# Optimization experiments

Hardware: AMD Instinct MI355X
Metric: run time of the kernel (lower is better)

The kernel has to match this reference:

```python
import jax, jax.numpy as jnp
import numpy as np


def setup_inputs() -> dict:
    key = jax.random.key(0)
    B, C, H, W = 8, 512, 64, 64
    x = jax.random.normal(key, (B, C, H, W), dtype=jnp.float32)
    # flag: 1 = masked (hole) position, 0 = known. Center-square hole as in
    # mask to this resolution; with shift_sz=1, mask_thred=1 flag == mask).
    flag = np.zeros((H, W), dtype=np.int32)
    flag[H // 4: 3 * H // 4, W // 4: 3 * W // 4] = 1
    return {"input": x, "flag": jnp.asarray(flag)}


def reference(input, flag):
    B, C, H, W = input.shape
    c2 = C // 2
    hw = H * W
    former = input[:, :c2]          # decoder features (B, c2, H, W)
    latter = input[:, c2:]          # encoder features (B, c2, H, W)

    ff = former.reshape(B, c2, hw)  # (B, c2, P)
    lf = latter.reshape(B, c2, hw)  # (B, c2, P)

    # L2-normalize latter pixel features (shift_sz=1 patches == pixels);
    # matches util.cosine_similarity's normalized conv kernels.
    norms = jnp.linalg.norm(lf, axis=1, keepdims=True)
    lnorm = lf / jnp.maximum(norms, 1e-8)

    # cosine[b, p, q] = <former[b,:,p], normed_latter[b,:,q]> for all positions;
    # masked q are excluded from the argmax (equiv. to gathering only the
    # non-mask patches via nonmask_point_idx, but jit-friendly fixed shapes).
    cos = jnp.einsum('bcp,bcq->bpq', ff, lnorm)
    flag_f = flag.reshape(hw)
    neg_inf = jnp.asarray(-jnp.inf, cos.dtype)
    cos = jnp.where(flag_f[None, None, :] == 1, neg_inf, cos)

    idx = jnp.argmax(cos, axis=2)   # (B, P): best non-mask source per position

    # Gather RAW latter features at best-match positions (util.shift_offsets
    # applies the 0/1 transition matrix ind_lst to the un-normalized latter).
    gidx = jnp.broadcast_to(idx[:, None, :], (B, c2, hw))
    shift = jnp.take_along_axis(lf, gidx, axis=2)            # (B, c2, P)
    shift = jnp.where(flag_f[None, None, :] == 1, shift, 0.0)  # zeros at known px
    shift = shift.reshape(B, c2, H, W)

    return jnp.concatenate([former, latter, shift], axis=1)   # (B, 3*c2, H, W)
```

## Files before the change

kernel.cpp:

```cpp
#include <hip/hip_runtime.h>
#include <stdint.h>
#include <math.h>

#define HW   4096
#define NB   8
#define NC   512
#define C2   256
#define PT   32
#define QC   512

#define WS_PACKED 0
#define WS_INVN   262144
#define WS_Q0     393216
#define WS_P1     409600
#define WS_CNT    425984
#define WS_IDX    427008
#define WS_INVC   558080

__device__ __forceinline__ unsigned long long mkkey(float v, unsigned q) {
    unsigned u = __float_as_uint(v);
    u = (u & 0x80000000u) ? ~u : (u | 0x80000000u);
    return ((unsigned long long)u << 32) | (unsigned long long)(0xFFFFFFFFu - q);
}

__device__ __forceinline__ float* lfc_region(float* out, int b) {
    return out + ((size_t)b * 768 + 512) * HW;
}

__global__ void compact_kernel(const int* __restrict__ flag, int* __restrict__ q0,
                               int* __restrict__ p1, int* __restrict__ cnt) {
    __shared__ int c1s[256];
    int t = threadIdx.x;
    int f[16]; int n1 = 0;
    #pragma unroll
    for (int j = 0; j < 16; ++j) { f[j] = flag[t*16 + j]; n1 += (f[j] == 1); }
    c1s[t] = n1;
    __syncthreads();
    if (t == 0) {
        int run = 0;
        for (int i = 0; i < 256; ++i) { int v = c1s[i]; c1s[i] = run; run += v; }
        cnt[0] = run;
        cnt[1] = HW - run;
    }
    __syncthreads();
    int b1 = c1s[t];
    int b0 = t*16 - c1s[t];
    for (int j = 0; j < 16; ++j) {
        int i = t*16 + j;
        if (f[j] == 1) p1[b1++] = i; else q0[b0++] = i;
    }
}

__global__ void norm_kernel(const float* __restrict__ x, float* __restrict__ invn) {
    int b = blockIdx.y;
    int q = blockIdx.x * 256 + threadIdx.x;
    const float* lf = x + ((size_t)b * NC + C2) * HW + q;
    float s = 0.f;
    #pragma unroll 8
    for (int c = 0; c < C2; ++c) {
        float v = lf[c * HW];
        s = fmaf(v, v, s);
    }
    invn[b * HW + q] = 1.0f / fmaxf(sqrtf(s), 1e-8f);
}

__global__ void pack_kernel(const float* __restrict__ x, const float* __restrict__ invn,
                            const int* __restrict__ q0, const int* __restrict__ cnt,
                            float* __restrict__ out, float* __restrict__ invc) {
    int b = blockIdx.z, c = blockIdx.y;
    int n0 = cnt[1];
    int ns = (n0 + 3) & ~3;
    int k = blockIdx.x * 256 + threadIdx.x;
    if (k >= n0) return;
    int q = q0[k];
    float* lfc = lfc_region(out, b);
    lfc[(size_t)c * ns + k] = x[((size_t)b * NC + C2 + c) * HW + q];
    if (c == 0) invc[b * HW + k] = invn[b * HW + q];
}

__global__ void __launch_bounds__(256) argmax_kernel(
        const float* __restrict__ x, float* __restrict__ out,
        const float* __restrict__ invc,
        const int* __restrict__ q0, const int* __restrict__ p1,
        const int* __restrict__ cnt, unsigned long long* __restrict__ packed) {
    int tile  = blockIdx.x;
    int chunk = blockIdx.y;
    int b     = blockIdx.z;
    int n1 = cnt[0], n0 = cnt[1];
    if (tile * PT >= n1) return;
    if (chunk * QC >= n0) return;
    int ns = (n0 + 3) & ~3;

    __shared__ float sff[256][PT];
    __shared__ int   sp[PT];

    int t = threadIdx.x;
    if (t < PT) sp[t] = (tile * PT + t < n1) ? p1[tile * PT + t] : -1;
    __syncthreads();

    const float* xb = x + (size_t)b * NC * HW;
    #pragma unroll
    for (int k = 0; k < 32; ++k) {
        int i = t + (k << 8);
        int c = i >> 5, j = i & 31;
        int p = sp[j];
        sff[c][j] = (p >= 0) ? xb[c * HW + p] : 0.f;
    }
    __syncthreads();

    int tp = t >> 6;
    int tq = t & 63;
    const float* lfc = lfc_region(out, b);
    int kbase = chunk * QC + tq * 4;

    const float* r = lfc + kbase;
    float4 bv0 = *(const float4*)(r);
    float4 bv1 = *(const float4*)(r + 256);
    r += ns;

    float acc[8][8];
    #pragma unroll
    for (int pi = 0; pi < 8; ++pi)
        #pragma unroll
        for (int j = 0; j < 8; ++j) acc[pi][j] = 0.f;

    #pragma unroll 2
    for (int c = 0; c < 255; ++c) {
        float4 nb0 = *(const float4*)(r);
        float4 nb1 = *(const float4*)(r + 256);
        r += ns;
        const float4* arow = (const float4*)&sff[c][tp * 8];
        float4 a0 = arow[0], a1 = arow[1];
        float av[8] = {a0.x, a0.y, a0.z, a0.w, a1.x, a1.y, a1.z, a1.w};
        float bv[8] = {bv0.x, bv0.y, bv0.z, bv0.w, bv1.x, bv1.y, bv1.z, bv1.w};
        #pragma unroll
        for (int pi = 0; pi < 8; ++pi)
            #pragma unroll
            for (int j = 0; j < 8; ++j)
                acc[pi][j] = fmaf(av[pi], bv[j], acc[pi][j]);
        bv0 = nb0; bv1 = nb1;
    }
    {
        const float4* arow = (const float4*)&sff[255][tp * 8];
        float4 a0 = arow[0], a1 = arow[1];
        float av[8] = {a0.x, a0.y, a0.z, a0.w, a1.x, a1.y, a1.z, a1.w};
        float bv[8] = {bv0.x, bv0.y, bv0.z, bv0.w, bv1.x, bv1.y, bv1.z, bv1.w};
        #pragma unroll
        for (int pi = 0; pi < 8; ++pi)
            #pragma unroll
            for (int j = 0; j < 8; ++j)
                acc[pi][j] = fmaf(av[pi], bv[j], acc[pi][j]);
    }

    float best[8];
    int   bq[8];
    #pragma unroll
    for (int pi = 0; pi < 8; ++pi) { best[pi] = -INFINITY; bq[pi] = 0x7FFFFFFF; }

    #pragma unroll
    for (int j = 0; j < 8; ++j) {
        int k = kbase + ((j < 4) ? j : 256 + (j - 4));
        if (k >= n0) continue;
        float sc = invc[b * HW + k];
        int   q  = q0[k];
        #pragma unroll
        for (int pi = 0; pi < 8; ++pi) {
            float cv = acc[pi][j] * sc;
            if (cv > best[pi] || (cv == best[pi] && q < bq[pi])) {
                best[pi] = cv; bq[pi] = q;
            }
        }
    }

    #pragma unroll
    for (int m = 1; m < 64; m <<= 1) {
        #pragma unroll
        for (int pi = 0; pi < 8; ++pi) {
            float ov = __shfl_xor(best[pi], m);
            int   oq = __shfl_xor(bq[pi], m);
            if (ov > best[pi] || (ov == best[pi] && oq < bq[pi])) {
                best[pi] = ov; bq[pi] = oq;
            }
        }
    }
    if (tq == 0) {
        #pragma unroll
        for (int pi = 0; pi < 8; ++pi) {
            int pidx = tile * PT + tp * 8 + pi;
            int p = (pidx < n1) ? p1[pidx] : -1;
            if (p >= 0)
                atomicMax(&packed[(size_t)b * HW + p], mkkey(best[pi], (unsigned)bq[pi]));
        }
    }
}

__global__ void decode_kernel(const unsigned long long* __restrict__ packed,
                              const int* __restrict__ flag, int* __restrict__ idx) {
    int b = blockIdx.y, p = blockIdx.x * 256 + threadIdx.x;
    int q = 0;
    if (flag[p] == 1) {
        unsigned low = (unsigned)(packed[(size_t)b * HW + p] & 0xFFFFFFFFull);
        q = (int)((0xFFFFFFFFu - low) & (HW - 1));
    }
    idx[b * HW + p] = q;
}

__global__ void copy_kernel(const float4* __restrict__ x4, float4* __restrict__ out4) {
    size_t i = (size_t)blockIdx.x * 256 + threadIdx.x;
    if (i >= (size_t)NB * NC * (HW / 4)) return;
    size_t p4 = i & 1023;
    size_t c  = (i >> 10) & 511;
    size_t b  = i >> 19;
    out4[(b * 768 + c) * 1024 + p4] = x4[i];
}

__global__ void shift_kernel(const float* __restrict__ x, const int* __restrict__ flag,
                             const int* __restrict__ idx, float* __restrict__ out) {
    int cc = blockIdx.x, b = blockIdx.y;
    const float* lfrow = x + ((size_t)b * NC + C2 + cc) * HW;
    float*       orow  = out + ((size_t)b * 768 + 512 + cc) * HW;
    const int*   idxb  = idx + b * HW;
    for (int p = threadIdx.x; p < HW; p += 256) {
        float v = 0.f;
        if (flag[p] == 1) v = lfrow[idxb[p]];
        orow[p] = v;
    }
}

extern "C" void kernel_launch(void* const* d_in, const int* in_sizes, int n_in,
                              void* d_out, int out_size, void* d_ws, size_t ws_size,
                              hipStream_t stream) {
    const float* x    = (const float*)d_in[0];
    const int*   flag = (const int*)d_in[1];
    float*       out  = (float*)d_out;
    char*        ws   = (char*)d_ws;

    unsigned long long* packed = (unsigned long long*)(ws + WS_PACKED);
    float* invn = (float*)(ws + WS_INVN);
    int*   q0   = (int*)(ws + WS_Q0);
    int*   p1   = (int*)(ws + WS_P1);
    int*   cnt  = (int*)(ws + WS_CNT);
    int*   idx  = (int*)(ws + WS_IDX);
    float* invc = (float*)(ws + WS_INVC);

    hipMemsetAsync(packed, 0, (size_t)NB * HW * sizeof(unsigned long long), stream);

    compact_kernel<<<1, 256, 0, stream>>>(flag, q0, p1, cnt);
    norm_kernel<<<dim3(HW / 256, NB), 256, 0, stream>>>(x, invn);
    pack_kernel<<<dim3(HW / 256, C2, NB), 256, 0, stream>>>(x, invn, q0, cnt, out, invc);
    copy_kernel<<<(NB * NC * (HW / 4) + 255) / 256, 256, 0, stream>>>((const float4*)x, (float4*)out);
    argmax_kernel<<<dim3(HW / PT, HW / QC, NB), 256, 0, stream>>>(x, out, invc, q0, p1, cnt, packed);
    decode_kernel<<<dim3(HW / 256, NB), 256, 0, stream>>>(packed, flag, idx);
    shift_kernel<<<dim3(C2, NB), 256, 0, stream>>>(x, flag, idx, out);
}
```

Before: 288.0 us.

## Pre-pack masked former features and shrink argmax tile to 8x4 per thread

Adds a pack_ff kernel that gathers the former features at masked positions into a compacted buffer placed in the output scratch region. The argmax kernel then fills shared memory with float4 loads from that buffer instead of doing scattered gathers from x. The kernel now stages channels in two halves of 128, which halves shared memory per block. The per-thread register tile drops from 8x8 to 8x4 and QC from 512 to 256, giving more blocks and lower register pressure, at the cost of less reuse of each B load and an extra launch plus traffic.

```diff
diff --git a/kernel.cpp b/kernel.cpp
--- a/kernel.cpp
+++ b/kernel.cpp
@@ -7,7 +7,7 @@
 #define NC   512
 #define C2   256
 #define PT   32
-#define QC   512
+#define QC   256
 
 #define WS_PACKED 0
 #define WS_INVN   262144
@@ -64,9 +64,9 @@
     invn[b * HW + q] = 1.0f / fmaxf(sqrtf(s), 1e-8f);
 }
 
-__global__ void pack_kernel(const float* __restrict__ x, const float* __restrict__ invn,
-                            const int* __restrict__ q0, const int* __restrict__ cnt,
-                            float* __restrict__ out, float* __restrict__ invc) {
+__global__ void pack_lf_kernel(const float* __restrict__ x, const float* __restrict__ invn,
+                               const int* __restrict__ q0, const int* __restrict__ cnt,
+                               float* __restrict__ out, float* __restrict__ invc) {
     int b = blockIdx.z, c = blockIdx.y;
     int n0 = cnt[1];
     int ns = (n0 + 3) & ~3;
@@ -78,9 +78,19 @@
     if (c == 0) invc[b * HW + k] = invn[b * HW + q];
 }
 
+__global__ void pack_ff_kernel(const float* __restrict__ x, const int* __restrict__ p1,
+                               const int* __restrict__ cnt, float* __restrict__ out) {
+    int b = blockIdx.z, c = blockIdx.y;
+    int n1 = cnt[0], n0 = cnt[1];
+    int ns = (n0 + 3) & ~3, ms = (n1 + 3) & ~3;
+    int m = blockIdx.x * 256 + threadIdx.x;
+    if (m >= n1) return;
+    float* ffc = lfc_region(out, b) + (size_t)C2 * ns;
+    ffc[(size_t)c * ms + m] = x[((size_t)b * NC + c) * HW + p1[m]];
+}
+
 __global__ void __launch_bounds__(256) argmax_kernel(
-        const float* __restrict__ x, float* __restrict__ out,
-        const float* __restrict__ invc,
+        float* __restrict__ out, const float* __restrict__ invc,
         const int* __restrict__ q0, const int* __restrict__ p1,
         const int* __restrict__ cnt, unsigned long long* __restrict__ packed) {
     int tile  = blockIdx.x;
@@ -89,67 +99,74 @@
     int n1 = cnt[0], n0 = cnt[1];
     if (tile * PT >= n1) return;
     if (chunk * QC >= n0) return;
-    int ns = (n0 + 3) & ~3;
-
-    __shared__ float sff[256][PT];
-    __shared__ int   sp[PT];
+    int ns = (n0 + 3) & ~3, ms = (n1 + 3) & ~3;
+
+    __shared__ float sff[128][PT];
 
     int t = threadIdx.x;
-    if (t < PT) sp[t] = (tile * PT + t < n1) ? p1[tile * PT + t] : -1;
-    __syncthreads();
-
-    const float* xb = x + (size_t)b * NC * HW;
-    #pragma unroll
-    for (int k = 0; k < 32; ++k) {
-        int i = t + (k << 8);
-        int c = i >> 5, j = i & 31;
-        int p = sp[j];
-        sff[c][j] = (p >= 0) ? xb[c * HW + p] : 0.f;
-    }
-    __syncthreads();
-
     int tp = t >> 6;
     int tq = t & 63;
+
     const float* lfc = lfc_region(out, b);
+    const float* ffc = lfc + (size_t)C2 * ns;
     int kbase = chunk * QC + tq * 4;
 
     const float* r = lfc + kbase;
-    float4 bv0 = *(const float4*)(r);
-    float4 bv1 = *(const float4*)(r + 256);
-    r += ns;
-
-    float acc[8][8];
+    float4 bv = *(const float4*)r;
+
+    float acc[8][4];
     #pragma unroll
     for (int pi = 0; pi < 8; ++pi)
         #pragma unroll
-        for (int j = 0; j < 8; ++j) acc[pi][j] = 0.f;
-
-    #pragma unroll 2
-    for (int c = 0; c < 255; ++c) {
-        float4 nb0 = *(const float4*)(r);
-        float4 nb1 = *(const float4*)(r + 256);
-        r += ns;
-        const float4* arow = (const float4*)&sff[c][tp * 8];
-        float4 a0 = arow[0], a1 = arow[1];
-        float av[8] = {a0.x, a0.y, a0.z, a0.w, a1.x, a1.y, a1.z, a1.w};
-        float bv[8] = {bv0.x, bv0.y, bv0.z, bv0.w, bv1.x, bv1.y, bv1.z, bv1.w};
-        #pragma unroll
-        for (int pi = 0; pi < 8; ++pi)
+        for (int j = 0; j < 4; ++j) acc[pi][j] = 0.f;
+
+    bool fulltile = (tile * PT + PT <= n1);
+
+    for (int h = 0; h < 2; ++h) {
+        __syncthreads();
+        if (fulltile) {
             #pragma unroll
-            for (int j = 0; j < 8; ++j)
-                acc[pi][j] = fmaf(av[pi], bv[j], acc[pi][j]);
-        bv0 = nb0; bv1 = nb1;
-    }
-    {
-        const float4* arow = (const float4*)&sff[255][tp * 8];
-        float4 a0 = arow[0], a1 = arow[1];
-        float av[8] = {a0.x, a0.y, a0.z, a0.w, a1.x, a1.y, a1.z, a1.w};
-        float bv[8] = {bv0.x, bv0.y, bv0.z, bv0.w, bv1.x, bv1.y, bv1.z, bv1.w};
-        #pragma unroll
-        for (int pi = 0; pi < 8; ++pi)
+            for (int k = 0; k < 4; ++k) {
+                int i4 = t + (k << 8);
+                int c = i4 >> 3, jg = i4 & 7;
+                ((float4*)sff)[i4] =
+                    *(const float4*)&ffc[(size_t)(h * 128 + c) * ms + tile * PT + jg * 4];
+            }
+        } else {
             #pragma unroll
-            for (int j = 0; j < 8; ++j)
-                acc[pi][j] = fmaf(av[pi], bv[j], acc[pi][j]);
+            for (int k = 0; k < 4; ++k) {
+                int i4 = t + (k << 8);
+                int c = i4 >> 3, jg = i4 & 7;
+                const float* src = &ffc[(size_t)(h * 128 + c) * ms];
+                int m0 = tile * PT + jg * 4;
+                float4 v;
+                v.x = (m0 + 0 < n1) ? src[m0 + 0] : 0.f;
+                v.y = (m0 + 1 < n1) ? src[m0 + 1] : 0.f;
+                v.z = (m0 + 2 < n1) ? src[m0 + 2] : 0.f;
+                v.w = (m0 + 3 < n1) ? src[m0 + 3] : 0.f;
+                ((float4*)sff)[i4] = v;
+            }
+        }
+        __syncthreads();
+
+        #pragma unroll 2
+        for (int cc = 0; cc < 128; ++cc) {
+            int cglob = h * 128 + cc;
+            const float* prow = (cglob < 255) ? (r + ns) : r;
+            float4 nb = *(const float4*)prow;
+            const float4* arow = (const float4*)&sff[cc][tp * 8];
+            float4 a0 = arow[0], a1 = arow[1];
+            float av[8] = {a0.x, a0.y, a0.z, a0.w, a1.x, a1.y, a1.z, a1.w};
+            #pragma unroll
+            for (int pi = 0; pi < 8; ++pi) {
+                acc[pi][0] = fmaf(av[pi], bv.x, acc[pi][0]);
+                acc[pi][1] = fmaf(av[pi], bv.y, acc[pi][1]);
+                acc[pi][2] = fmaf(av[pi], bv.z, acc[pi][2]);
+                acc[pi][3] = fmaf(av[pi], bv.w, acc[pi][3]);
+            }
+            bv = nb;
+            r = prow;
+        }
     }
 
     float best[8];
@@ -158,8 +175,8 @@
     for (int pi = 0; pi < 8; ++pi) { best[pi] = -INFINITY; bq[pi] = 0x7FFFFFFF; }
 
     #pragma unroll
-    for (int j = 0; j < 8; ++j) {
-        int k = kbase + ((j < 4) ? j : 256 + (j - 4));
+    for (int j = 0; j < 4; ++j) {
+        int k = kbase + j;
         if (k >= n0) continue;
         float sc = invc[b * HW + k];
         int   q  = q0[k];
@@ -247,9 +264,10 @@
 
     compact_kernel<<<1, 256, 0, stream>>>(flag, q0, p1, cnt);
     norm_kernel<<<dim3(HW / 256, NB), 256, 0, stream>>>(x, invn);
-    pack_kernel<<<dim3(HW / 256, C2, NB), 256, 0, stream>>>(x, invn, q0, cnt, out, invc);
+    pack_lf_kernel<<<dim3(HW / 256, C2, NB), 256, 0, stream>>>(x, invn, q0, cnt, out, invc);
+    pack_ff_kernel<<<dim3(HW / 256, C2, NB), 256, 0, stream>>>(x, p1, cnt, out);
     copy_kernel<<<(NB * NC * (HW / 4) + 255) / 256, 256, 0, stream>>>((const float4*)x, (float4*)out);
-    argmax_kernel<<<dim3(HW / PT, HW / QC, NB), 256, 0, stream>>>(x, out, invc, q0, p1, cnt, packed);
+    argmax_kernel<<<dim3(HW / PT, HW / QC, NB), 256, 0, stream>>>(out, invc, q0, p1, cnt, packed);
     decode_kernel<<<dim3(HW / 256, NB), 256, 0, stream>>>(packed, flag, idx);
     shift_kernel<<<dim3(C2, NB), 256, 0, stream>>>(x, flag, idx, out);
 }
```

Result: no change. 288.2 us (+0.1%).
